# Kernel optimization log

Hardware: AMD Instinct MI355X
Metric: run time of the kernel (lower is better)

The kernel has to match this reference:

```python
import jax, jax.numpy as jnp
import numpy as np

NEG = 0.01  # LeakyReLU negative_slope
N_NODES = 100000
N_EDGES = 400000
D = 128
IN_CH = 16
EDGE_DIM = 1


def _linear(x, w, b):
    # torch.nn.Linear convention: y = x @ W^T + b, W: [out, in]
    return x @ w.T + b


def setup_inputs() -> dict:
    key = jax.random.key(0)
    ks = jax.random.split(key, 32)

    def W(k, o, i):
        return jax.random.normal(k, (o, i), dtype=jnp.float32) * 0.02

    def B(k, o):
        return jax.random.normal(k, (o,), dtype=jnp.float32) * 0.02

    return {
        "x": jax.random.normal(ks[0], (N_NODES, IN_CH), dtype=jnp.float32),
        "edge_index": jax.random.randint(ks[1], (2, N_EDGES), 0, N_NODES, dtype=jnp.int64),
        "edge_weight": jax.random.uniform(ks[2], (N_EDGES, EDGE_DIM), dtype=jnp.float32),
        # prep MLP: in_ch -> 128 (LeakyReLU) -> 128 (Tanh)
        "prep_w0": W(ks[3], D, IN_CH), "prep_b0": B(ks[4], D),
        "prep_w1": W(ks[5], D, D), "prep_b1": B(ks[6], D),
        # GINEConv edge lin: edge_dim -> 128
        "edge_w": W(ks[7], D, EDGE_DIM), "edge_b": B(ks[8], D),
        # GINEConv nn: 128 -> 128 (LReLU) -> 128 (LReLU) -> 128 (Tanh)
        "mlp_w0": W(ks[9], D, D), "mlp_b0": B(ks[10], D),
        "mlp_w1": W(ks[11], D, D), "mlp_b1": B(ks[12], D),
        "mlp_w2": W(ks[13], D, D), "mlp_b2": B(ks[14], D),
        # post MLP: (128+128) -> 128 (LReLU) -> 64 (Tanh)
        "post_w0": W(ks[15], D, 2 * D), "post_b0": B(ks[16], D),
        "post_w1": W(ks[17], 64, D), "post_b1": B(ks[18], 64),
    }


def reference(x, edge_index, edge_weight,
              prep_w0, prep_b0, prep_w1, prep_b1,
              edge_w, edge_b,
              mlp_w0, mlp_b0, mlp_w1, mlp_b1, mlp_w2, mlp_b2,
              post_w0, post_b0, post_w1, post_b1):
    lrelu = lambda v: jax.nn.leaky_relu(v, negative_slope=NEG)
    n = x.shape[0]

    # sequential_prep
    h = lrelu(_linear(x, prep_w0, prep_b0))
    h = jnp.tanh(_linear(h, prep_w1, prep_b1))  # [N, D]

    r = h  # skip connection (x.clone())

    # GINEConv: message = relu(x_j + lin(edge_attr)); aggr = sum per dst
    e = _linear(edge_weight, edge_w, edge_b)            # [E, D]
    m = jax.nn.relu(h[edge_index[0]] + e)               # gather + edge add
    agg = jax.ops.segment_sum(m, edge_index[1], num_segments=n)  # scatter-sum
    z = h + agg  # (1 + eps) * x_i + aggr, eps = 0
    z = lrelu(_linear(z, mlp_w0, mlp_b0))
    z = lrelu(_linear(z, mlp_w1, mlp_b1))
    z = jnp.tanh(_linear(z, mlp_w2, mlp_b2))            # [N, D]

    # skip-cat
    h2 = jnp.concatenate([z, r], axis=1)                # [N, 2D]

    # sequential_post
    o = lrelu(_linear(h2, post_w0, post_b0))
    o = jnp.tanh(_linear(o, post_w1, post_b1))          # [N, 64]
    return o
```

## Files before the change

kernel.cpp:

```cpp
#include <hip/hip_runtime.h>

typedef short bf16x8 __attribute__((ext_vector_type(8)));
typedef float f32x4 __attribute__((ext_vector_type(4)));

#define LDP 136
#define LDX 40
#define NEG 0.01f

__device__ __forceinline__ unsigned short f2bf(float f) {
  union { float f; unsigned u; } v; v.f = f;
  unsigned u = v.u;
  return (unsigned short)((u + 0x7fffu + ((u >> 16) & 1u)) >> 16);
}
__device__ __forceinline__ unsigned pack2(float a, float b) {
  return ((unsigned)f2bf(b) << 16) | (unsigned)f2bf(a);
}
__device__ __forceinline__ float bflo(unsigned u) { return __uint_as_float(u << 16); }
__device__ __forceinline__ float bfhi(unsigned u) { return __uint_as_float(u & 0xffff0000u); }

__device__ __forceinline__ float lrelu(float v) {
  return fmaxf(v, 0.0f) + NEG * fminf(v, 0.0f);
}
__device__ __forceinline__ float tanh_fast(float x) {
  float e = __expf(2.0f * x);
  return 1.0f - __fdividef(2.0f, e + 1.0f);
}

template<int COLS>
__device__ __forceinline__ void stage_w(const float* __restrict__ g, int gld,
                                        unsigned short* s, int lds, int rows, int tid) {
  const int perRow = COLS / 4;
  const int total = rows * perRow;
  for (int i = tid; i < total; i += 256) {
    int r = i / perRow, q = i - r * perRow;
    float4 v = *(const float4*)(g + r * gld + q * 4);
    ushort4 o; o.x = f2bf(v.x); o.y = f2bf(v.y); o.z = f2bf(v.z); o.w = f2bf(v.w);
    *(ushort4*)(s + r * lds + q * 4) = o;
  }
}

__device__ __forceinline__ void stage_bf(const unsigned short* __restrict__ g,
                                         unsigned short* s, int rows, int tid) {
  const int total = rows * 16;
  for (int i = tid; i < total; i += 256) {
    int r = i >> 4, q = i & 15;
    *(uint4*)(s + r * LDP + q * 8) = *(const uint4*)(g + r * 128 + q * 8);
  }
}

template<int MF, int NF>
__device__ __forceinline__ void zero_acc(f32x4 acc[MF][NF]) {
  #pragma unroll
  for (int m = 0; m < MF; ++m)
    #pragma unroll
    for (int n = 0; n < NF; ++n) {
      f32x4 z = {0.f, 0.f, 0.f, 0.f};
      acc[m][n] = z;
    }
}

template<int MF, int NF, int KSTEPS, int LDB>
__device__ __forceinline__ void wave_gemm(const unsigned short* wS, const unsigned short* bS,
                                          int chBase, int nodeBase, f32x4 acc[MF][NF], int lane) {
  const int l15 = lane & 15, lg = lane >> 4;
  #pragma unroll
  for (int ks = 0; ks < KSTEPS; ++ks) {
    const int k = ks * 32 + lg * 8;
    bf16x8 a[MF], b[NF];
    #pragma unroll
    for (int mf = 0; mf < MF; ++mf)
      a[mf] = *(const bf16x8*)(wS + (chBase + 16 * mf + l15) * LDP + k);
    #pragma unroll
    for (int nf = 0; nf < NF; ++nf)
      b[nf] = *(const bf16x8*)(bS + (nodeBase + 16 * nf + l15) * LDB + k);
    #pragma unroll
    for (int mf = 0; mf < MF; ++mf)
      #pragma unroll
      for (int nf = 0; nf < NF; ++nf)
        acc[mf][nf] = __builtin_amdgcn_mfma_f32_16x16x32_bf16(a[mf], b[nf], acc[mf][nf], 0, 0, 0);
  }
}

template<int ACT>
__device__ __forceinline__ void write_act_lds_T(f32x4 acc[4][4], const float* __restrict__ bias,
                                                unsigned short* aS, int chBase, int nodeBase,
                                                int l15, int lg) {
  #pragma unroll
  for (int mf = 0; mf < 4; ++mf) {
    const int ch4 = chBase + 16 * mf + 4 * lg;
    const float4 bv = *(const float4*)(bias + ch4);
    #pragma unroll
    for (int nf = 0; nf < 4; ++nf) {
      const int node = nodeBase + 16 * nf + l15;
      float v0 = acc[mf][nf][0] + bv.x;
      float v1 = acc[mf][nf][1] + bv.y;
      float v2 = acc[mf][nf][2] + bv.z;
      float v3 = acc[mf][nf][3] + bv.w;
      if (ACT == 0) { v0 = lrelu(v0); v1 = lrelu(v1); v2 = lrelu(v2); v3 = lrelu(v3); }
      else { v0 = tanh_fast(v0); v1 = tanh_fast(v1); v2 = tanh_fast(v2); v3 = tanh_fast(v3); }
      uint2 o; o.x = pack2(v0, v1); o.y = pack2(v2, v3);
      *(uint2*)(aS + node * LDP + ch4) = o;
    }
  }
}

extern "C" __global__ void __launch_bounds__(256) wconv_kernel(
    const float* __restrict__ mw0, const float* __restrict__ mw1, const float* __restrict__ mw2,
    const float* __restrict__ qw0, const float* __restrict__ qw1,
    unsigned short* wbf, int* deg, int N) {
  int gid = blockIdx.x * 256 + threadIdx.x;
  if (gid < 22528) {
    int f = gid;
    float4 v;
    if (f < 12288) {
      const float* m = (f < 4096) ? mw0 : ((f < 8192) ? mw1 : mw2);
      v = *(const float4*)(m + (size_t)(f & 4095) * 4);
    } else if (f < 20480) {
      int g = f - 12288; int half = g >> 12; int r = (g & 4095) >> 5, q = g & 31;
      v = *(const float4*)(qw0 + r * 256 + half * 128 + q * 4);
    } else {
      int g = f - 20480;
      v = *(const float4*)(qw1 + g * 4);
    }
    ushort4 o; o.x = f2bf(v.x); o.y = f2bf(v.y); o.z = f2bf(v.z); o.w = f2bf(v.w);
    *(ushort4*)(wbf + gid * 4) = o;
  }
  if (gid < N) deg[gid] = 0;
}

extern "C" __global__ void __launch_bounds__(256, 2) prep_kernel(
    const float* __restrict__ x,
    const float* __restrict__ w0, const float* __restrict__ b0,
    const float* __restrict__ w1, const float* __restrict__ b1,
    const int* __restrict__ ei, int* deg, int E,
    unsigned short* hB, int N) {
  __shared__ unsigned short xS[128 * LDX];
  __shared__ unsigned short aS[128 * LDP];
  __shared__ unsigned short wS[128 * LDP];
  const int tid = threadIdx.x, lane = tid & 63, wave = tid >> 6;
  const int l15 = lane & 15, lg = lane >> 4;
  const int wr = wave >> 1, wc = wave & 1;
  const int chBase = 64 * wr, nodeBase = 64 * wc;
  const int nb = blockIdx.x * 128;

  for (int i = tid; i < 128 * 4; i += 256) {
    int r = i >> 2, q = i & 3;
    int node = nb + r; node = node < N ? node : N - 1;
    float4 v = *(const float4*)(x + node * 16 + q * 4);
    ushort4 o; o.x = f2bf(v.x); o.y = f2bf(v.y); o.z = f2bf(v.z); o.w = f2bf(v.w);
    *(ushort4*)(xS + r * LDX + q * 4) = o;
    ushort4 zz; zz.x = 0; zz.y = 0; zz.z = 0; zz.w = 0;
    *(ushort4*)(xS + r * LDX + 16 + q * 4) = zz;
  }
  stage_w<16>(w0, 16, wS, LDP, 128, tid);
  for (int i = tid; i < 128 * 4; i += 256) {
    int r = i >> 2, q = i & 3;
    ushort4 zz; zz.x = 0; zz.y = 0; zz.z = 0; zz.w = 0;
    *(ushort4*)(wS + r * LDP + 16 + q * 4) = zz;
  }
  for (int e = blockIdx.x * 256 + tid; e < E; e += gridDim.x * 256)
    atomicAdd(&deg[ei[E + e]], 1);
  __syncthreads();

  f32x4 acc[4][4];
  zero_acc<4, 4>(acc);
  wave_gemm<4, 4, 1, LDX>(wS, xS, chBase, nodeBase, acc, lane);
  __syncthreads();
  write_act_lds_T<0>(acc, b0, aS, chBase, nodeBase, l15, lg);
  stage_w<128>(w1, 128, wS, LDP, 128, tid);
  __syncthreads();

  zero_acc<4, 4>(acc);
  wave_gemm<4, 4, 4, LDP>(wS, aS, chBase, nodeBase, acc, lane);
  #pragma unroll
  for (int mf = 0; mf < 4; ++mf) {
    const int ch4 = chBase + 16 * mf + 4 * lg;
    const float4 bv = *(const float4*)(b1 + ch4);
    #pragma unroll
    for (int nf = 0; nf < 4; ++nf) {
      const int node = nb + nodeBase + 16 * nf + l15;
      if (node < N) {
        float v0 = tanh_fast(acc[mf][nf][0] + bv.x);
        float v1 = tanh_fast(acc[mf][nf][1] + bv.y);
        float v2 = tanh_fast(acc[mf][nf][2] + bv.z);
        float v3 = tanh_fast(acc[mf][nf][3] + bv.w);
        uint2 o; o.x = pack2(v0, v1); o.y = pack2(v2, v3);
        *(uint2*)(hB + (size_t)node * 128 + ch4) = o;
      }
    }
  }
}

extern "C" __global__ void __launch_bounds__(256) scan_partials_kernel(
    const int* __restrict__ deg, int* partials, int N) {
  __shared__ int red[256];
  int b = blockIdx.x, t = threadIdx.x;
  int base = b * 2048 + t * 8, s = 0;
  #pragma unroll
  for (int i = 0; i < 8; ++i) { int idx = base + i; s += (idx < N) ? deg[idx] : 0; }
  red[t] = s; __syncthreads();
  for (int off = 128; off > 0; off >>= 1) {
    if (t < off) red[t] += red[t + off];
    __syncthreads();
  }
  if (t == 0) partials[b] = red[0];
}

extern "C" __global__ void scan_base_kernel(const int* __restrict__ partials, int* basearr, int nb) {
  int lane = threadIdx.x;
  int orig = (lane < nb) ? partials[lane] : 0;
  int v = orig;
  #pragma unroll
  for (int off = 1; off < 64; off <<= 1) {
    int u = __shfl_up(v, off);
    if (lane >= off) v += u;
  }
  if (lane < nb) basearr[lane] = v - orig;
}

extern "C" __global__ void __launch_bounds__(256) scan_apply_kernel(
    const int* __restrict__ deg, const int* __restrict__ basearr,
    int* offs, int* cur, int N) {
  __shared__ int sc[256];
  int b = blockIdx.x, t = threadIdx.x;
  int base = b * 2048 + t * 8;
  int loc[8], s = 0;
  #pragma unroll
  for (int i = 0; i < 8; ++i) { int idx = base + i; loc[i] = (idx < N) ? deg[idx] : 0; s += loc[i]; }
  sc[t] = s; __syncthreads();
  for (int off = 1; off < 256; off <<= 1) {
    int v = sc[t];
    int u = (t >= off) ? sc[t - off] : 0;
    __syncthreads();
    sc[t] = v + u;
    __syncthreads();
  }
  int run = basearr[b] + ((t == 0) ? 0 : sc[t - 1]);
  #pragma unroll
  for (int i = 0; i < 8; ++i) {
    int idx = base + i;
    if (idx < N) { offs[idx] = run; cur[idx] = run; run += loc[i]; }
  }
}

extern "C" __global__ void __launch_bounds__(256) scatter_kernel(
    const int* __restrict__ ei, const float* __restrict__ ew,
    int* cur, int2* recs, int E) {
  int e = blockIdx.x * 256 + threadIdx.x;
  if (e < E) {
    int dst = ei[E + e];
    int slot = atomicAdd(&cur[dst], 1);
    int2 r; r.x = ei[e]; r.y = __float_as_int(ew[e]);
    recs[slot] = r;
  }
}

extern "C" __global__ void __launch_bounds__(256) agg_kernel(
    const int* __restrict__ offs, const int* __restrict__ cur,
    const int2* __restrict__ recs,
    const float* __restrict__ elw, const float* __restrict__ elb,
    const unsigned short* __restrict__ hB, unsigned short* zB, int N) {
  const int lane = threadIdx.x & 63, wv = threadIdx.x >> 6;
  const int node = blockIdx.x * 4 + wv;
  if (node >= N) return;
  const float2 wl = *(const float2*)(elw + 2 * lane);
  const float2 bl = *(const float2*)(elb + 2 * lane);
  const int s = offs[node], epos = cur[node];
  float c0 = 0.f, c1 = 0.f;
  for (int j = s; j < epos; ++j) {
    int2 rec = recs[j];
    float w = __int_as_float(rec.y);
    unsigned hv = *(const unsigned*)(hB + (size_t)rec.x * 128 + 2 * lane);
    c0 += fmaxf(bflo(hv) + w * wl.x + bl.x, 0.0f);
    c1 += fmaxf(bfhi(hv) + w * wl.y + bl.y, 0.0f);
  }
  unsigned hself = *(const unsigned*)(hB + (size_t)node * 128 + 2 * lane);
  float z0v = bflo(hself) + c0, z1v = bfhi(hself) + c1;
  *(unsigned*)(zB + (size_t)node * 128 + 2 * lane) = pack2(z0v, z1v);
}

extern "C" __global__ void __launch_bounds__(256, 2) node_kernel(
    const unsigned short* __restrict__ zB, const unsigned short* __restrict__ hB,
    const unsigned short* __restrict__ wbf,
    const float* __restrict__ mb0, const float* __restrict__ mb1, const float* __restrict__ mb2,
    const float* __restrict__ qb0, const float* __restrict__ qb1,
    float* out, int N) {
  __shared__ unsigned short aS[128 * LDP];
  __shared__ unsigned short wS[128 * LDP];
  const int tid = threadIdx.x, lane = tid & 63, wave = tid >> 6;
  const int l15 = lane & 15, lg = lane >> 4;
  const int wr = wave >> 1, wc = wave & 1;
  const int chBase = 64 * wr, nodeBase = 64 * wc;
  const int nb = blockIdx.x * 128;

  for (int i = tid; i < 128 * 16; i += 256) {
    int r = i >> 4, q = i & 15;
    int node = nb + r; node = node < N ? node : N - 1;
    *(uint4*)(aS + r * LDP + q * 8) = *(const uint4*)(zB + (size_t)node * 128 + q * 8);
  }
  stage_bf(wbf, wS, 128, tid);
  __syncthreads();

  f32x4 acc[4][4];

  zero_acc<4, 4>(acc);
  wave_gemm<4, 4, 4, LDP>(wS, aS, chBase, nodeBase, acc, lane);
  __syncthreads();
  write_act_lds_T<0>(acc, mb0, aS, chBase, nodeBase, l15, lg);
  stage_bf(wbf + 16384, wS, 128, tid);
  __syncthreads();

  zero_acc<4, 4>(acc);
  wave_gemm<4, 4, 4, LDP>(wS, aS, chBase, nodeBase, acc, lane);
  __syncthreads();
  write_act_lds_T<0>(acc, mb1, aS, chBase, nodeBase, l15, lg);
  stage_bf(wbf + 32768, wS, 128, tid);
  __syncthreads();

  zero_acc<4, 4>(acc);
  wave_gemm<4, 4, 4, LDP>(wS, aS, chBase, nodeBase, acc, lane);
  __syncthreads();
  write_act_lds_T<1>(acc, mb2, aS, chBase, nodeBase, l15, lg);
  stage_bf(wbf + 49152, wS, 128, tid);
  __syncthreads();

  zero_acc<4, 4>(acc);
  wave_gemm<4, 4, 4, LDP>(wS, aS, chBase, nodeBase, acc, lane);
  __syncthreads();
  for (int i = tid; i < 128 * 16; i += 256) {
    int r = i >> 4, q = i & 15;
    int node = nb + r; node = node < N ? node : N - 1;
    *(uint4*)(aS + r * LDP + q * 8) = *(const uint4*)(hB + (size_t)node * 128 + q * 8);
  }
  stage_bf(wbf + 65536, wS, 128, tid);
  __syncthreads();
  wave_gemm<4, 4, 4, LDP>(wS, aS, chBase, nodeBase, acc, lane);
  __syncthreads();
  write_act_lds_T<0>(acc, qb0, aS, chBase, nodeBase, l15, lg);
  stage_bf(wbf + 81920, wS, 64, tid);
  __syncthreads();

  f32x4 acc2[2][4];
  zero_acc<2, 4>(acc2);
  wave_gemm<2, 4, 4, LDP>(wS, aS, 32 * wr, nodeBase, acc2, lane);
  #pragma unroll
  for (int mf = 0; mf < 2; ++mf) {
    const int ch4 = 32 * wr + 16 * mf + 4 * lg;
    const float4 bv = *(const float4*)(qb1 + ch4);
    #pragma unroll
    for (int nf = 0; nf < 4; ++nf) {
      const int node = nb + nodeBase + 16 * nf + l15;
      if (node < N) {
        float4 o;
        o.x = tanh_fast(acc2[mf][nf][0] + bv.x);
        o.y = tanh_fast(acc2[mf][nf][1] + bv.y);
        o.z = tanh_fast(acc2[mf][nf][2] + bv.z);
        o.w = tanh_fast(acc2[mf][nf][3] + bv.w);
        *(float4*)(out + (size_t)node * 64 + ch4) = o;
      }
    }
  }
}

extern "C" void kernel_launch(void* const* d_in, const int* in_sizes, int n_in,
                              void* d_out, int out_size, void* d_ws, size_t ws_size,
                              hipStream_t stream) {
  const float* x   = (const float*)d_in[0];
  const int*   ei  = (const int*)d_in[1];
  const float* ew  = (const float*)d_in[2];
  const float* pw0 = (const float*)d_in[3];
  const float* pb0 = (const float*)d_in[4];
  const float* pw1 = (const float*)d_in[5];
  const float* pb1 = (const float*)d_in[6];
  const float* elw = (const float*)d_in[7];
  const float* elb = (const float*)d_in[8];
  const float* mw0 = (const float*)d_in[9];
  const float* mb0 = (const float*)d_in[10];
  const float* mw1 = (const float*)d_in[11];
  const float* mb1 = (const float*)d_in[12];
  const float* mw2 = (const float*)d_in[13];
  const float* mb2 = (const float*)d_in[14];
  const float* qw0 = (const float*)d_in[15];
  const float* qb0 = (const float*)d_in[16];
  const float* qw1 = (const float*)d_in[17];
  const float* qb1 = (const float*)d_in[18];
  float* out = (float*)d_out;

  const int N = in_sizes[0] / 16;
  const int E = in_sizes[1] / 2;

  char* p = (char*)d_ws;
  auto alloc = [&](size_t bytes) { char* r = p; p += (bytes + 255) & ~(size_t)255; return r; };
  const size_t hB_bytes = (size_t)N * 128 * 2;

  unsigned short* zB   = (unsigned short*)alloc(hB_bytes);
  int2*           recs = (int2*)alloc((size_t)E * 8);
  int*            deg  = (int*)alloc((size_t)N * 4);
  int*            offs = (int*)alloc((size_t)N * 4);
  int*            cur  = (int*)alloc((size_t)N * 4);
  int*            part = (int*)alloc(256 * 4);
  int*            basearr = (int*)alloc(256 * 4);
  unsigned short* wbf  = (unsigned short*)alloc(90112 * 2);

  unsigned short* hB;
  if ((size_t)(p - (char*)d_ws) + hB_bytes <= ws_size) {
    hB = (unsigned short*)alloc(hB_bytes);
  } else {
    hB = (unsigned short*)d_out;
  }

  const int nblk  = (N + 127) / 128;
  const int nb1   = (N + 2047) / 2048;
  const int eblk  = (E + 255) / 256;
  const int wconv_threads = (N > 22528) ? N : 22528;

  wconv_kernel<<<dim3((wconv_threads + 255) / 256), dim3(256), 0, stream>>>(
      mw0, mw1, mw2, qw0, qw1, wbf, deg, N);
  prep_kernel<<<dim3(nblk), dim3(256), 0, stream>>>(x, pw0, pb0, pw1, pb1, ei, deg, E, hB, N);
  scan_partials_kernel<<<dim3(nb1), dim3(256), 0, stream>>>(deg, part, N);
  scan_base_kernel<<<dim3(1), dim3(64), 0, stream>>>(part, basearr, nb1);
  scan_apply_kernel<<<dim3(nb1), dim3(256), 0, stream>>>(deg, basearr, offs, cur, N);
  scatter_kernel<<<dim3(eblk), dim3(256), 0, stream>>>(ei, ew, cur, recs, E);
  agg_kernel<<<dim3((N + 3) / 4), dim3(256), 0, stream>>>(offs, cur, recs, elw, elb, hB, zB, N);
  node_kernel<<<dim3(nblk), dim3(256), 0, stream>>>(zB, hB, wbf, mb0, mb1, mb2, qb0, qb1, out, N);
}
```

Before: 287.4 us.

## Restructure node MLPs into persistent kernels with LDS-resident swizzled bf16 weights

Pre-packs every weight matrix once into XOR-swizzled bf16 tiles, including the prep-layer weights. The prep and node kernels become persistent grids of 256 blocks that keep the full weight set resident in LDS and loop over node tiles, each wave handling a 32-node strip with per-wave scratch instead of block-wide syncs. Node activations are stored in the same swizzled row layout, the aggregation loop is unrolled by four, and the node MLP is split into two kernels linked by an extra z3 buffer. This aims to remove repeated weight staging, bank conflicts and barriers, at the cost of an extra global round trip for z3 and large LDS use per block.

After: 424.0 us. 1.48x slower.

```diff
diff --git a/kernel.cpp b/kernel.cpp
--- a/kernel.cpp
+++ b/kernel.cpp
@@ -3,9 +3,16 @@
 typedef short bf16x8 __attribute__((ext_vector_type(8)));
 typedef float f32x4 __attribute__((ext_vector_type(4)));
 
-#define LDP 136
-#define LDX 40
 #define NEG 0.01f
+
+#define OFF_P0 0
+#define OFF_P1 8192
+#define OFF_M0 40960
+#define OFF_M1 73728
+#define OFF_M2 106496
+#define OFF_Q0 139264
+#define OFF_Q1 204800
+#define WBF_BYTES 221184
 
 __device__ __forceinline__ unsigned short f2bf(float f) {
   union { float f; unsigned u; } v; v.f = f;
@@ -17,177 +24,173 @@
 }
 __device__ __forceinline__ float bflo(unsigned u) { return __uint_as_float(u << 16); }
 __device__ __forceinline__ float bfhi(unsigned u) { return __uint_as_float(u & 0xffff0000u); }
-
-__device__ __forceinline__ float lrelu(float v) {
-  return fmaxf(v, 0.0f) + NEG * fminf(v, 0.0f);
-}
+__device__ __forceinline__ float lrelu(float v) { return fmaxf(v, 0.0f) + NEG * fminf(v, 0.0f); }
 __device__ __forceinline__ float tanh_fast(float x) {
   float e = __expf(2.0f * x);
   return 1.0f - __fdividef(2.0f, e + 1.0f);
 }
 
-template<int COLS>
-__device__ __forceinline__ void stage_w(const float* __restrict__ g, int gld,
-                                        unsigned short* s, int lds, int rows, int tid) {
-  const int perRow = COLS / 4;
-  const int total = rows * perRow;
-  for (int i = tid; i < total; i += 256) {
-    int r = i / perRow, q = i - r * perRow;
-    float4 v = *(const float4*)(g + r * gld + q * 4);
-    ushort4 o; o.x = f2bf(v.x); o.y = f2bf(v.y); o.z = f2bf(v.z); o.w = f2bf(v.w);
-    *(ushort4*)(s + r * lds + q * 4) = o;
-  }
-}
-
-__device__ __forceinline__ void stage_bf(const unsigned short* __restrict__ g,
-                                         unsigned short* s, int rows, int tid) {
-  const int total = rows * 16;
-  for (int i = tid; i < total; i += 256) {
-    int r = i >> 4, q = i & 15;
-    *(uint4*)(s + r * LDP + q * 8) = *(const uint4*)(g + r * 128 + q * 8);
-  }
-}
-
-template<int MF, int NF>
-__device__ __forceinline__ void zero_acc(f32x4 acc[MF][NF]) {
-  #pragma unroll
-  for (int m = 0; m < MF; ++m)
-    #pragma unroll
-    for (int n = 0; n < NF; ++n) {
-      f32x4 z = {0.f, 0.f, 0.f, 0.f};
-      acc[m][n] = z;
-    }
-}
-
-template<int MF, int NF, int KSTEPS, int LDB>
-__device__ __forceinline__ void wave_gemm(const unsigned short* wS, const unsigned short* bS,
-                                          int chBase, int nodeBase, f32x4 acc[MF][NF], int lane) {
-  const int l15 = lane & 15, lg = lane >> 4;
-  #pragma unroll
-  for (int ks = 0; ks < KSTEPS; ++ks) {
-    const int k = ks * 32 + lg * 8;
-    bf16x8 a[MF], b[NF];
-    #pragma unroll
-    for (int mf = 0; mf < MF; ++mf)
-      a[mf] = *(const bf16x8*)(wS + (chBase + 16 * mf + l15) * LDP + k);
-    #pragma unroll
-    for (int nf = 0; nf < NF; ++nf)
-      b[nf] = *(const bf16x8*)(bS + (nodeBase + 16 * nf + l15) * LDB + k);
-    #pragma unroll
-    for (int mf = 0; mf < MF; ++mf)
-      #pragma unroll
-      for (int nf = 0; nf < NF; ++nf)
-        acc[mf][nf] = __builtin_amdgcn_mfma_f32_16x16x32_bf16(a[mf], b[nf], acc[mf][nf], 0, 0, 0);
+
+__device__ __forceinline__ void zacc82(f32x4 acc[8][2]) {
+  #pragma unroll
+  for (int m = 0; m < 8; ++m)
+    #pragma unroll
+    for (int n = 0; n < 2; ++n) { f32x4 z = {0.f,0.f,0.f,0.f}; acc[m][n] = z; }
+}
+
+__device__ __forceinline__ void gemm128(const char* wbase, const bf16x8 b[2][4],
+                                        f32x4 acc[8][2], int l15, int lg) {
+  #pragma unroll
+  for (int ks = 0; ks < 4; ++ks)
+    #pragma unroll
+    for (int mf = 0; mf < 8; ++mf) {
+      const int row = 16*mf + l15;
+      bf16x8 a = *(const bf16x8*)(wbase + row*256 + ((16*lg + 64*ks) ^ ((row&7)<<4)));
+      acc[mf][0] = __builtin_amdgcn_mfma_f32_16x16x32_bf16(a, b[0][ks], acc[mf][0], 0,0,0);
+      acc[mf][1] = __builtin_amdgcn_mfma_f32_16x16x32_bf16(a, b[1][ks], acc[mf][1], 0,0,0);
+    }
+}
+
+__device__ __forceinline__ void read_bfrags(const char* scr, bf16x8 b[2][4], int l15, int lg) {
+  #pragma unroll
+  for (int nf = 0; nf < 2; ++nf) {
+    const int n = 16*nf + l15;
+    #pragma unroll
+    for (int ks = 0; ks < 4; ++ks)
+      b[nf][ks] = *(const bf16x8*)(scr + n*256 + ((16*lg + 64*ks) ^ ((n&7)<<4)));
+  }
+}
+
+__device__ __forceinline__ void ep_lds(const f32x4 acc[8][2], const float* __restrict__ bias,
+                                       char* scr, int l15, int lg) {
+  #pragma unroll
+  for (int mf = 0; mf < 8; ++mf) {
+    const int ch4 = 16*mf + 4*lg;
+    const float4 bv = *(const float4*)(bias + ch4);
+    #pragma unroll
+    for (int nf = 0; nf < 2; ++nf) {
+      const int n = 16*nf + l15;
+      float v0 = lrelu(acc[mf][nf][0]+bv.x), v1 = lrelu(acc[mf][nf][1]+bv.y);
+      float v2 = lrelu(acc[mf][nf][2]+bv.z), v3 = lrelu(acc[mf][nf][3]+bv.w);
+      uint2 o = { pack2(v0,v1), pack2(v2,v3) };
+      *(uint2*)(scr + n*256 + ((32*mf + 8*lg) ^ ((n&7)<<4))) = o;
+    }
   }
 }
 
 template<int ACT>
-__device__ __forceinline__ void write_act_lds_T(f32x4 acc[4][4], const float* __restrict__ bias,
-                                                unsigned short* aS, int chBase, int nodeBase,
-                                                int l15, int lg) {
-  #pragma unroll
-  for (int mf = 0; mf < 4; ++mf) {
-    const int ch4 = chBase + 16 * mf + 4 * lg;
+__device__ __forceinline__ void ep_glb(const f32x4 acc[8][2], const float* __restrict__ bias,
+                                       char* dst, int strip, int N, int l15, int lg) {
+  #pragma unroll
+  for (int mf = 0; mf < 8; ++mf) {
+    const int ch4 = 16*mf + 4*lg;
     const float4 bv = *(const float4*)(bias + ch4);
     #pragma unroll
-    for (int nf = 0; nf < 4; ++nf) {
-      const int node = nodeBase + 16 * nf + l15;
-      float v0 = acc[mf][nf][0] + bv.x;
-      float v1 = acc[mf][nf][1] + bv.y;
-      float v2 = acc[mf][nf][2] + bv.z;
-      float v3 = acc[mf][nf][3] + bv.w;
-      if (ACT == 0) { v0 = lrelu(v0); v1 = lrelu(v1); v2 = lrelu(v2); v3 = lrelu(v3); }
-      else { v0 = tanh_fast(v0); v1 = tanh_fast(v1); v2 = tanh_fast(v2); v3 = tanh_fast(v3); }
-      uint2 o; o.x = pack2(v0, v1); o.y = pack2(v2, v3);
-      *(uint2*)(aS + node * LDP + ch4) = o;
-    }
-  }
-}
-
-extern "C" __global__ void __launch_bounds__(256) wconv_kernel(
+    for (int nf = 0; nf < 2; ++nf) {
+      const int node = strip + 16*nf + l15;
+      if (node < N) {
+        float v0 = acc[mf][nf][0]+bv.x, v1 = acc[mf][nf][1]+bv.y;
+        float v2 = acc[mf][nf][2]+bv.z, v3 = acc[mf][nf][3]+bv.w;
+        if (ACT == 0) { v0=lrelu(v0); v1=lrelu(v1); v2=lrelu(v2); v3=lrelu(v3); }
+        else { v0=tanh_fast(v0); v1=tanh_fast(v1); v2=tanh_fast(v2); v3=tanh_fast(v3); }
+        uint2 o = { pack2(v0,v1), pack2(v2,v3) };
+        *(uint2*)(dst + (size_t)node*256 + ((32*mf + 8*lg) ^ ((node&7)<<4))) = o;
+      }
+    }
+  }
+}
+
+extern "C" __global__ void __launch_bounds__(256) wpack_kernel(
+    const float* __restrict__ pw0, const float* __restrict__ pw1,
     const float* __restrict__ mw0, const float* __restrict__ mw1, const float* __restrict__ mw2,
     const float* __restrict__ qw0, const float* __restrict__ qw1,
-    unsigned short* wbf, int* deg, int N) {
+    char* wbf, int* deg, int N) {
   int gid = blockIdx.x * 256 + threadIdx.x;
-  if (gid < 22528) {
-    int f = gid;
-    float4 v;
-    if (f < 12288) {
-      const float* m = (f < 4096) ? mw0 : ((f < 8192) ? mw1 : mw2);
-      v = *(const float4*)(m + (size_t)(f & 4095) * 4);
-    } else if (f < 20480) {
-      int g = f - 12288; int half = g >> 12; int r = (g & 4095) >> 5, q = g & 31;
-      v = *(const float4*)(qw0 + r * 256 + half * 128 + q * 4);
-    } else {
-      int g = f - 20480;
-      v = *(const float4*)(qw1 + g * 4);
-    }
-    ushort4 o; o.x = f2bf(v.x); o.y = f2bf(v.y); o.z = f2bf(v.z); o.w = f2bf(v.w);
-    *(ushort4*)(wbf + gid * 4) = o;
+  if (gid < 13824) {
+    int c = gid;
+    const float* src = nullptr;
+    int dstB = 0;
+    bool zero = false;
+    if (c < 512) { int r = c >> 2, q = c & 3;
+      dstB = OFF_P0 + r*64 + ((q*16) ^ ((r&3)<<4));
+      if (q < 2) src = pw0 + r*16 + q*8; else zero = true;
+    } else if (c < 2560) { int i = c - 512, r = i >> 4, q = i & 15;
+      dstB = OFF_P1 + r*256 + ((q*16) ^ ((r&7)<<4));
+      src = pw1 + r*128 + q*8;
+    } else if (c < 8704) { int i = c - 2560, sl = i >> 11, j = i & 2047, r = j >> 4, q = j & 15;
+      const float* m = (sl==0) ? mw0 : ((sl==1) ? mw1 : mw2);
+      dstB = OFF_M0 + sl*32768 + r*256 + ((q*16) ^ ((r&7)<<4));
+      src = m + r*128 + q*8;
+    } else if (c < 12800) { int i = c - 8704, r = i >> 5, q = i & 31;
+      dstB = OFF_Q0 + r*512 + ((q*16) ^ ((r&7)<<4));
+      src = qw0 + r*256 + q*8;
+    } else { int i = c - 12800, r = i >> 4, q = i & 15;
+      dstB = OFF_Q1 + r*256 + ((q*16) ^ ((r&7)<<4));
+      src = qw1 + r*128 + q*8;
+    }
+    ushort4 lo, hi;
+    if (zero) { lo.x=lo.y=lo.z=lo.w=0; hi.x=hi.y=hi.z=hi.w=0; }
+    else {
+      float4 a = *(const float4*)src, b = *(const float4*)(src + 4);
+      lo.x=f2bf(a.x); lo.y=f2bf(a.y); lo.z=f2bf(a.z); lo.w=f2bf(a.w);
+      hi.x=f2bf(b.x); hi.y=f2bf(b.y); hi.z=f2bf(b.z); hi.w=f2bf(b.w);
+    }
+    *(ushort4*)(wbf + dstB) = lo;
+    *(ushort4*)(wbf + dstB + 8) = hi;
   }
   if (gid < N) deg[gid] = 0;
 }
 
-extern "C" __global__ void __launch_bounds__(256, 2) prep_kernel(
+extern "C" __global__ void __launch_bounds__(512, 2) prep_kernel(
     const float* __restrict__ x,
-    const float* __restrict__ w0, const float* __restrict__ b0,
-    const float* __restrict__ w1, const float* __restrict__ b1,
+    const float* __restrict__ pb0, const float* __restrict__ pb1,
+    const char* __restrict__ wbf,
     const int* __restrict__ ei, int* deg, int E,
-    unsigned short* hB, int N) {
-  __shared__ unsigned short xS[128 * LDX];
-  __shared__ unsigned short aS[128 * LDP];
-  __shared__ unsigned short wS[128 * LDP];
-  const int tid = threadIdx.x, lane = tid & 63, wave = tid >> 6;
+    char* hB, int N, int ntiles) {
+  __shared__ char wP[40960];
+  __shared__ char scr_all[8*8192];
+  const int tid = threadIdx.x, lane = tid & 63, wv = tid >> 6;
   const int l15 = lane & 15, lg = lane >> 4;
-  const int wr = wave >> 1, wc = wave & 1;
-  const int chBase = 64 * wr, nodeBase = 64 * wc;
-  const int nb = blockIdx.x * 128;
-
-  for (int i = tid; i < 128 * 4; i += 256) {
-    int r = i >> 2, q = i & 3;
-    int node = nb + r; node = node < N ? node : N - 1;
-    float4 v = *(const float4*)(x + node * 16 + q * 4);
-    ushort4 o; o.x = f2bf(v.x); o.y = f2bf(v.y); o.z = f2bf(v.z); o.w = f2bf(v.w);
-    *(ushort4*)(xS + r * LDX + q * 4) = o;
-    ushort4 zz; zz.x = 0; zz.y = 0; zz.z = 0; zz.w = 0;
-    *(ushort4*)(xS + r * LDX + 16 + q * 4) = zz;
-  }
-  stage_w<16>(w0, 16, wS, LDP, 128, tid);
-  for (int i = tid; i < 128 * 4; i += 256) {
-    int r = i >> 2, q = i & 3;
-    ushort4 zz; zz.x = 0; zz.y = 0; zz.z = 0; zz.w = 0;
-    *(ushort4*)(wS + r * LDP + 16 + q * 4) = zz;
-  }
-  for (int e = blockIdx.x * 256 + tid; e < E; e += gridDim.x * 256)
+
+  for (int i = tid; i < 2560; i += 512)
+    *(uint4*)(wP + i*16) = *(const uint4*)(wbf + OFF_P0 + i*16);
+  for (int e = blockIdx.x*512 + tid; e < E; e += gridDim.x*512)
     atomicAdd(&deg[ei[E + e]], 1);
   __syncthreads();
-
-  f32x4 acc[4][4];
-  zero_acc<4, 4>(acc);
-  wave_gemm<4, 4, 1, LDX>(wS, xS, chBase, nodeBase, acc, lane);
-  __syncthreads();
-  write_act_lds_T<0>(acc, b0, aS, chBase, nodeBase, l15, lg);
-  stage_w<128>(w1, 128, wS, LDP, 128, tid);
-  __syncthreads();
-
-  zero_acc<4, 4>(acc);
-  wave_gemm<4, 4, 4, LDP>(wS, aS, chBase, nodeBase, acc, lane);
-  #pragma unroll
-  for (int mf = 0; mf < 4; ++mf) {
-    const int ch4 = chBase + 16 * mf + 4 * lg;
-    const float4 bv = *(const float4*)(b1 + ch4);
-    #pragma unroll
-    for (int nf = 0; nf < 4; ++nf) {
-      const int node = nb + nodeBase + 16 * nf + l15;
-      if (node < N) {
-        float v0 = tanh_fast(acc[mf][nf][0] + bv.x);
-        float v1 = tanh_fast(acc[mf][nf][1] + bv.y);
-        float v2 = tanh_fast(acc[mf][nf][2] + bv.z);
-        float v3 = tanh_fast(acc[mf][nf][3] + bv.w);
-        uint2 o; o.x = pack2(v0, v1); o.y = pack2(v2, v3);
-        *(uint2*)(hB + (size_t)node * 128 + ch4) = o;
-      }
-    }
+  char* scr = scr_all + wv*8192;
+
+  for (int tile = blockIdx.x; tile < ntiles; tile += gridDim.x) {
+    const int strip = tile*256 + wv*32;
+    bf16x8 bx[2];
+    #pragma unroll
+    for (int nf = 0; nf < 2; ++nf) {
+      int node = strip + 16*nf + l15; node = node < N ? node : N-1;
+      if (lg < 2) {
+        float4 u = *(const float4*)(x + (size_t)node*16 + lg*8);
+        float4 v = *(const float4*)(x + (size_t)node*16 + lg*8 + 4);
+        bf16x8 t;
+        t[0]=(short)f2bf(u.x); t[1]=(short)f2bf(u.y); t[2]=(short)f2bf(u.z); t[3]=(short)f2bf(u.w);
+        t[4]=(short)f2bf(v.x); t[5]=(short)f2bf(v.y); t[6]=(short)f2bf(v.z); t[7]=(short)f2bf(v.w);
+        bx[nf] = t;
+      } else {
+        bf16x8 t = {0,0,0,0,0,0,0,0}; bx[nf] = t;
+      }
+    }
+    f32x4 acc[8][2];
+    zacc82(acc);
+    #pragma unroll
+    for (int mf = 0; mf < 8; ++mf) {
+      const int row = 16*mf + l15;
+      bf16x8 a = *(const bf16x8*)(wP + row*64 + ((16*lg) ^ ((row&3)<<4)));
+      acc[mf][0] = __builtin_amdgcn_mfma_f32_16x16x32_bf16(a, bx[0], acc[mf][0], 0,0,0);
+      acc[mf][1] = __builtin_amdgcn_mfma_f32_16x16x32_bf16(a, bx[1], acc[mf][1], 0,0,0);
+    }
+    ep_lds(acc, pb0, scr, l15, lg);
+    bf16x8 b1[2][4];
+    read_bfrags(scr, b1, l15, lg);
+    zacc82(acc);
+    gemm128(wP + OFF_P1, b1, acc, l15, lg);
+    ep_glb<1>(acc, pb1, hB, strip, N, l15, lg);
   }
 }
 
@@ -259,104 +262,168 @@
     const int* __restrict__ offs, const int* __restrict__ cur,
     const int2* __restrict__ recs,
     const float* __restrict__ elw, const float* __restrict__ elb,
-    const unsigned short* __restrict__ hB, unsigned short* zB, int N) {
+    const char* __restrict__ hB, char* zB, int N) {
   const int lane = threadIdx.x & 63, wv = threadIdx.x >> 6;
   const int node = blockIdx.x * 4 + wv;
   if (node >= N) return;
-  const float2 wl = *(const float2*)(elw + 2 * lane);
-  const float2 bl = *(const float2*)(elb + 2 * lane);
-  const int s = offs[node], epos = cur[node];
+  const float2 wl = *(const float2*)(elw + 2*lane);
+  const float2 bl = *(const float2*)(elb + 2*lane);
+  const int byteL = lane * 4;
+  const int s = offs[node], e = cur[node];
   float c0 = 0.f, c1 = 0.f;
-  for (int j = s; j < epos; ++j) {
-    int2 rec = recs[j];
-    float w = __int_as_float(rec.y);
-    unsigned hv = *(const unsigned*)(hB + (size_t)rec.x * 128 + 2 * lane);
-    c0 += fmaxf(bflo(hv) + w * wl.x + bl.x, 0.0f);
-    c1 += fmaxf(bfhi(hv) + w * wl.y + bl.y, 0.0f);
-  }
-  unsigned hself = *(const unsigned*)(hB + (size_t)node * 128 + 2 * lane);
-  float z0v = bflo(hself) + c0, z1v = bfhi(hself) + c1;
-  *(unsigned*)(zB + (size_t)node * 128 + 2 * lane) = pack2(z0v, z1v);
-}
-
-extern "C" __global__ void __launch_bounds__(256, 2) node_kernel(
-    const unsigned short* __restrict__ zB, const unsigned short* __restrict__ hB,
-    const unsigned short* __restrict__ wbf,
+  int j = s;
+  for (; j + 4 <= e; j += 4) {
+    int2 r0 = recs[j], r1 = recs[j+1], r2 = recs[j+2], r3 = recs[j+3];
+    unsigned u0 = *(const unsigned*)(hB + (size_t)r0.x*256 + (byteL ^ ((r0.x&7)<<4)));
+    unsigned u1 = *(const unsigned*)(hB + (size_t)r1.x*256 + (byteL ^ ((r1.x&7)<<4)));
+    unsigned u2 = *(const unsigned*)(hB + (size_t)r2.x*256 + (byteL ^ ((r2.x&7)<<4)));
+    unsigned u3 = *(const unsigned*)(hB + (size_t)r3.x*256 + (byteL ^ ((r3.x&7)<<4)));
+    float w0 = __int_as_float(r0.y), w1 = __int_as_float(r1.y);
+    float w2 = __int_as_float(r2.y), w3 = __int_as_float(r3.y);
+    c0 += fmaxf(bflo(u0) + w0*wl.x + bl.x, 0.f); c1 += fmaxf(bfhi(u0) + w0*wl.y + bl.y, 0.f);
+    c0 += fmaxf(bflo(u1) + w1*wl.x + bl.x, 0.f); c1 += fmaxf(bfhi(u1) + w1*wl.y + bl.y, 0.f);
+    c0 += fmaxf(bflo(u2) + w2*wl.x + bl.x, 0.f); c1 += fmaxf(bfhi(u2) + w2*wl.y + bl.y, 0.f);
+    c0 += fmaxf(bflo(u3) + w3*wl.x + bl.x, 0.f); c1 += fmaxf(bfhi(u3) + w3*wl.y + bl.y, 0.f);
+  }
+  for (; j < e; ++j) {
+    int2 r = recs[j];
+    unsigned u = *(const unsigned*)(hB + (size_t)r.x*256 + (byteL ^ ((r.x&7)<<4)));
+    float w = __int_as_float(r.y);
+    c0 += fmaxf(bflo(u) + w*wl.x + bl.x, 0.f);
+    c1 += fmaxf(bfhi(u) + w*wl.y + bl.y, 0.f);
+  }
+  unsigned hs = *(const unsigned*)(hB + (size_t)node*256 + (byteL ^ ((node&7)<<4)));
+  unsigned o = pack2(bflo(hs) + c0, bfhi(hs) + c1);
+  *(unsigned*)(zB + (size_t)node*256 + (byteL ^ ((node&7)<<4))) = o;
+}
+
+extern "C" __global__ void __launch_bounds__(384) nodeA_kernel(
+    const char* __restrict__ zB, const char* __restrict__ wbf,
     const float* __restrict__ mb0, const float* __restrict__ mb1, const float* __restrict__ mb2,
+    char* z3, int N, int ntiles) {
+  __shared__ char wM[98304];
+  __shared__ char scr_all[6*8192];
+  const int tid = threadIdx.x, lane = tid & 63, wv = tid >> 6;
+  const int l15 = lane & 15, lg = lane >> 4;
+
+  for (int i = tid; i < 6144; i += 384)
+    *(uint4*)(wM + i*16) = *(const uint4*)(wbf + OFF_M0 + i*16);
+  __syncthreads();
+  char* scr = scr_all + wv*8192;
+
+  for (int tile = blockIdx.x; tile < ntiles; tile += gridDim.x) {
+    const int strip = tile*192 + wv*32;
+    bf16x8 b0[2][4];
+    #pragma unroll
+    for (int nf = 0; nf < 2; ++nf) {
+      int node = strip + 16*nf + l15; node = node < N ? node : N-1;
+      const char* zr = zB + (size_t)node*256;
+      const int sw = (node&7) << 4;
+      #pragma unroll
+      for (int ks = 0; ks < 4; ++ks)
+        b0[nf][ks] = *(const bf16x8*)(zr + ((16*lg + 64*ks) ^ sw));
+    }
+    f32x4 acc[8][2];
+    zacc82(acc);
+    gemm128(wM, b0, acc, l15, lg);
+    ep_lds(acc, mb0, scr, l15, lg);
+
+    bf16x8 b1[2][4];
+    read_bfrags(scr, b1, l15, lg);
+    zacc82(acc);
+    gemm128(wM + 32768, b1, acc, l15, lg);
+    ep_lds(acc, mb1, scr, l15, lg);
+
+    bf16x8 b2[2][4];
+    read_bfrags(scr, b2, l15, lg);
+    zacc82(acc);
+    gemm128(wM + 65536, b2, acc, l15, lg);
+    ep_glb<1>(acc, mb2, z3, strip, N, l15, lg);
+  }
+}
+
+extern "C" __global__ void __launch_bounds__(384) nodeB_kernel(
+    const char* __restrict__ z3, const char* __restrict__ hB, const char* __restrict__ wbf,
     const float* __restrict__ qb0, const float* __restrict__ qb1,
-    float* out, int N) {
-  __shared__ unsigned short aS[128 * LDP];
-  __shared__ unsigned short wS[128 * LDP];
-  const int tid = threadIdx.x, lane = tid & 63, wave = tid >> 6;
+    float* out, int N, int ntiles) {
+  __shared__ char wQ[81920];
+  __shared__ char scr_all[6*8192];
+  const int tid = threadIdx.x, lane = tid & 63, wv = tid >> 6;
   const int l15 = lane & 15, lg = lane >> 4;
-  const int wr = wave >> 1, wc = wave & 1;
-  const int chBase = 64 * wr, nodeBase = 64 * wc;
-  const int nb = blockIdx.x * 128;
-
-  for (int i = tid; i < 128 * 16; i += 256) {
-    int r = i >> 4, q = i & 15;
-    int node = nb + r; node = node < N ? node : N - 1;
-    *(uint4*)(aS + r * LDP + q * 8) = *(const uint4*)(zB + (size_t)node * 128 + q * 8);
-  }
-  stage_bf(wbf, wS, 128, tid);
+
+  for (int i = tid; i < 5120; i += 384)
+    *(uint4*)(wQ + i*16) = *(const uint4*)(wbf + OFF_Q0 + i*16);
   __syncthreads();
-
-  f32x4 acc[4][4];
-
-  zero_acc<4, 4>(acc);
-  wave_gemm<4, 4, 4, LDP>(wS, aS, chBase, nodeBase, acc, lane);
-  __syncthreads();
-  write_act_lds_T<0>(acc, mb0, aS, chBase, nodeBase, l15, lg);
-  stage_bf(wbf + 16384, wS, 128, tid);
-  __syncthreads();
-
-  zero_acc<4, 4>(acc);
-  wave_gemm<4, 4, 4, LDP>(wS, aS, chBase, nodeBase, acc, lane);
-  __syncthreads();
-  write_act_lds_T<0>(acc, mb1, aS, chBase, nodeBase, l15, lg);
-  stage_bf(wbf + 32768, wS, 128, tid);
-  __syncthreads();
-
-  zero_acc<4, 4>(acc);
-  wave_gemm<4, 4, 4, LDP>(wS, aS, chBase, nodeBase, acc, lane);
-  __syncthreads();
-  write_act_lds_T<1>(acc, mb2, aS, chBase, nodeBase, l15, lg);
-  stage_bf(wbf + 49152, wS, 128, tid);
-  __syncthreads();
-
-  zero_acc<4, 4>(acc);
-  wave_gemm<4, 4, 4, LDP>(wS, aS, chBase, nodeBase, acc, lane);
-  __syncthreads();
-  for (int i = tid; i < 128 * 16; i += 256) {
-    int r = i >> 4, q = i & 15;
-    int node = nb + r; node = node < N ? node : N - 1;
-    *(uint4*)(aS + r * LDP + q * 8) = *(const uint4*)(hB + (size_t)node * 128 + q * 8);
-  }
-  stage_bf(wbf + 65536, wS, 128, tid);
-  __syncthreads();
-  wave_gemm<4, 4, 4, LDP>(wS, aS, chBase, nodeBase, acc, lane);
-  __syncthreads();
-  write_act_lds_T<0>(acc, qb0, aS, chBase, nodeBase, l15, lg);
-  stage_bf(wbf + 81920, wS, 64, tid);
-  __syncthreads();
-
-  f32x4 acc2[2][4];
-  zero_acc<2, 4>(acc2);
-  wave_gemm<2, 4, 4, LDP>(wS, aS, 32 * wr, nodeBase, acc2, lane);
-  #pragma unroll
-  for (int mf = 0; mf < 2; ++mf) {
-    const int ch4 = 32 * wr + 16 * mf + 4 * lg;
-    const float4 bv = *(const float4*)(qb1 + ch4);
-    #pragma unroll
-    for (int nf = 0; nf < 4; ++nf) {
-      const int node = nb + nodeBase + 16 * nf + l15;
-      if (node < N) {
-        float4 o;
-        o.x = tanh_fast(acc2[mf][nf][0] + bv.x);
-        o.y = tanh_fast(acc2[mf][nf][1] + bv.y);
-        o.z = tanh_fast(acc2[mf][nf][2] + bv.z);
-        o.w = tanh_fast(acc2[mf][nf][3] + bv.w);
-        *(float4*)(out + (size_t)node * 64 + ch4) = o;
+  char* scr = scr_all + wv*8192;
+
+  for (int tile = blockIdx.x; tile < ntiles; tile += gridDim.x) {
+    const int strip = tile*192 + wv*32;
+    bf16x8 bz[2][4], bh[2][4];
+    #pragma unroll
+    for (int nf = 0; nf < 2; ++nf) {
+      int node = strip + 16*nf + l15; node = node < N ? node : N-1;
+      const char* zr = z3 + (size_t)node*256;
+      const char* hr = hB + (size_t)node*256;
+      const int sw = (node&7) << 4;
+      #pragma unroll
+      for (int ks = 0; ks < 4; ++ks) {
+        bz[nf][ks] = *(const bf16x8*)(zr + ((16*lg + 64*ks) ^ sw));
+        bh[nf][ks] = *(const bf16x8*)(hr + ((16*lg + 64*ks) ^ sw));
+      }
+    }
+    f32x4 acc[8][2];
+    zacc82(acc);
+    #pragma unroll
+    for (int ks = 0; ks < 4; ++ks)
+      #pragma unroll
+      for (int mf = 0; mf < 8; ++mf) {
+        const int row = 16*mf + l15;
+        bf16x8 a = *(const bf16x8*)(wQ + row*512 + ((16*lg + 64*ks) ^ ((row&7)<<4)));
+        acc[mf][0] = __builtin_amdgcn_mfma_f32_16x16x32_bf16(a, bz[0][ks], acc[mf][0], 0,0,0);
+        acc[mf][1] = __builtin_amdgcn_mfma_f32_16x16x32_bf16(a, bz[1][ks], acc[mf][1], 0,0,0);
+      }
+    #pragma unroll
+    for (int ks = 0; ks < 4; ++ks)
+      #pragma unroll
+      for (int mf = 0; mf < 8; ++mf) {
+        const int row = 16*mf + l15;
+        bf16x8 a = *(const bf16x8*)(wQ + row*512 + ((16*lg + 64*(ks+4)) ^ ((row&7)<<4)));
+        acc[mf][0] = __builtin_amdgcn_mfma_f32_16x16x32_bf16(a, bh[0][ks], acc[mf][0], 0,0,0);
+        acc[mf][1] = __builtin_amdgcn_mfma_f32_16x16x32_bf16(a, bh[1][ks], acc[mf][1], 0,0,0);
+      }
+    ep_lds(acc, qb0, scr, l15, lg);
+
+    bf16x8 bt[2][4];
+    read_bfrags(scr, bt, l15, lg);
+    f32x4 a2[4][2];
+    #pragma unroll
+    for (int m = 0; m < 4; ++m)
+      #pragma unroll
+      for (int n = 0; n < 2; ++n) { f32x4 z = {0.f,0.f,0.f,0.f}; a2[m][n] = z; }
+    #pragma unroll
+    for (int ks = 0; ks < 4; ++ks)
+      #pragma unroll
+      for (int mf = 0; mf < 4; ++mf) {
+        const int row = 16*mf + l15;
+        bf16x8 a = *(const bf16x8*)(wQ + 65536 + row*256 + ((16*lg + 64*ks) ^ ((row&7)<<4)));
+        a2[mf][0] = __builtin_amdgcn_mfma_f32_16x16x32_bf16(a, bt[0][ks], a2[mf][0], 0,0,0);
+        a2[mf][1] = __builtin_amdgcn_mfma_f32_16x16x32_bf16(a, bt[1][ks], a2[mf][1], 0,0,0);
+      }
+    #pragma unroll
+    for (int mf = 0; mf < 4; ++mf) {
+      const int ch4 = 16*mf + 4*lg;
+      const float4 bv = *(const float4*)(qb1 + ch4);
+      #pragma unroll
+      for (int nf = 0; nf < 2; ++nf) {
+        const int node = strip + 16*nf + l15;
+        if (node < N) {
+          float4 o;
+          o.x = tanh_fast(a2[mf][nf][0] + bv.x);
+          o.y = tanh_fast(a2[mf][nf][1] + bv.y);
+          o.z = tanh_fast(a2[mf][nf][2] + bv.z);
+          o.w = tanh_fast(a2[mf][nf][3] + bv.w);
+          *(float4*)(out + (size_t)node*64 + ch4) = o;
+        }
       }
     }
   }
@@ -391,36 +458,39 @@
 
   char* p = (char*)d_ws;
   auto alloc = [&](size_t bytes) { char* r = p; p += (bytes + 255) & ~(size_t)255; return r; };
-  const size_t hB_bytes = (size_t)N * 128 * 2;
-
-  unsigned short* zB   = (unsigned short*)alloc(hB_bytes);
-  int2*           recs = (int2*)alloc((size_t)E * 8);
-  int*            deg  = (int*)alloc((size_t)N * 4);
-  int*            offs = (int*)alloc((size_t)N * 4);
-  int*            cur  = (int*)alloc((size_t)N * 4);
-  int*            part = (int*)alloc(256 * 4);
-  int*            basearr = (int*)alloc(256 * 4);
-  unsigned short* wbf  = (unsigned short*)alloc(90112 * 2);
-
-  unsigned short* hB;
-  if ((size_t)(p - (char*)d_ws) + hB_bytes <= ws_size) {
-    hB = (unsigned short*)alloc(hB_bytes);
+  const size_t rowBytes = (size_t)N * 256;
+
+  char* zB      = alloc(rowBytes);
+  char* z3      = alloc(rowBytes);
+  int2* recs    = (int2*)alloc((size_t)E * 8);
+  int*  deg     = (int*)alloc((size_t)N * 4);
+  int*  offs    = (int*)alloc((size_t)N * 4);
+  int*  cur     = (int*)alloc((size_t)N * 4);
+  int*  part    = (int*)alloc(256 * 4);
+  int*  basearr = (int*)alloc(256 * 4);
+  char* wbf     = alloc(WBF_BYTES);
+
+  char* hB;
+  if ((size_t)(p - (char*)d_ws) + rowBytes <= ws_size) {
+    hB = alloc(rowBytes);
   } else {
-    hB = (unsigned short*)d_out;
-  }
-
-  const int nblk  = (N + 127) / 128;
-  const int nb1   = (N + 2047) / 2048;
-  const int eblk  = (E + 255) / 256;
-  const int wconv_threads = (N > 22528) ? N : 22528;
-
-  wconv_kernel<<<dim3((wconv_threads + 255) / 256), dim3(256), 0, stream>>>(
-      mw0, mw1, mw2, qw0, qw1, wbf, deg, N);
-  prep_kernel<<<dim3(nblk), dim3(256), 0, stream>>>(x, pw0, pb0, pw1, pb1, ei, deg, E, hB, N);
+    hB = (char*)d_out;
+  }
+
+  const int ntilesP  = (N + 255) / 256;
+  const int ntilesAB = (N + 191) / 192;
+  const int nb1  = (N + 2047) / 2048;
+  const int eblk = (E + 255) / 256;
+  const int pgrid = ((13824 > N ? 13824 : N) + 255) / 256;
+
+  wpack_kernel<<<dim3(pgrid), dim3(256), 0, stream>>>(pw0, pw1, mw0, mw1, mw2, qw0, qw1,
+                                                      wbf, deg, N);
+  prep_kernel<<<dim3(256), dim3(512), 0, stream>>>(x, pb0, pb1, wbf, ei, deg, E, hB, N, ntilesP);
   scan_partials_kernel<<<dim3(nb1), dim3(256), 0, stream>>>(deg, part, N);
   scan_base_kernel<<<dim3(1), dim3(64), 0, stream>>>(part, basearr, nb1);
   scan_apply_kernel<<<dim3(nb1), dim3(256), 0, stream>>>(deg, basearr, offs, cur, N);
   scatter_kernel<<<dim3(eblk), dim3(256), 0, stream>>>(ei, ew, cur, recs, E);
   agg_kernel<<<dim3((N + 3) / 4), dim3(256), 0, stream>>>(offs, cur, recs, elw, elb, hB, zB, N);
-  node_kernel<<<dim3(nblk), dim3(256), 0, stream>>>(zB, hB, wbf, mb0, mb1, mb2, qb0, qb1, out, N);
-}
+  nodeA_kernel<<<dim3(256), dim3(384), 0, stream>>>(zB, wbf, mb0, mb1, mb2, z3, N, ntilesAB);
+  nodeB_kernel<<<dim3(256), dim3(384), 0, stream>>>(z3, hB, wbf, qb0, qb1, out, N, ntilesAB);
+}
```
